# Kernel optimization log

Measured on AMD Instinct MI355X. Metric: run time of the kernel, lower is better.

Reference implementation:

```python
import jax, jax.numpy as jnp
import numpy as np

BN_EPS = 1e-5


def setup_inputs() -> dict:
    key = jax.random.key(0)
    ks = jax.random.split(key, 8)
    B, C, N = 4, 256, 4096
    s = 1.0 / np.sqrt(C)
    return {
        "feature": jax.random.normal(ks[0], (B, C, N, 1), dtype=jnp.float32),
        "Wa": jax.random.normal(ks[1], (C, C), dtype=jnp.float32) * s,
        "ba": jnp.zeros((C,), dtype=jnp.float32),
        "Wb": jax.random.normal(ks[2], (C, C), dtype=jnp.float32) * s,
        "bb": jnp.zeros((C,), dtype=jnp.float32),
        "Wm": jax.random.normal(ks[3], (C, C), dtype=jnp.float32) * s,
        "bm": jnp.zeros((C,), dtype=jnp.float32),
        "gamma": jnp.ones((C,), dtype=jnp.float32),
        "beta": jnp.zeros((C,), dtype=jnp.float32),
        "rmean": jnp.zeros((C,), dtype=jnp.float32),
        "rvar": jnp.ones((C,), dtype=jnp.float32),
        "alpha": jnp.zeros((1,), dtype=jnp.float32),
    }


def reference(feature, Wa, ba, Wb, bb, Wm, bm, gamma, beta, rmean, rvar, alpha):
    # feature: [B, C, N, 1]; 1x1 convs are per-point linear maps over channels.
    x = feature[..., 0]  # [B, C, N]
    a = jnp.einsum('oc,bcn->bon', Wa, x) + ba[None, :, None]  # fc_a
    b = jnp.einsum('oc,bcn->bon', Wb, x) + bb[None, :, None]  # fc_b
    # att = softmax(a^T @ b) over last dim: [B, N, N]
    att = jax.nn.softmax(jnp.einsum('bcn,bcm->bnm', a, b), axis=2)
    # mlp: 1x1 conv + eval-mode BatchNorm
    m = jnp.einsum('oc,bcn->bon', Wm, x) + bm[None, :, None]
    inv = jax.lax.rsqrt(rvar + BN_EPS)
    m = (m - rmean[None, :, None]) * (inv * gamma)[None, :, None] + beta[None, :, None]
    # f = att @ m^T -> [B, N, C], back to [B, C, N]
    f = jnp.einsum('bnm,bcm->bcn', att, m)
    return feature + alpha[0] * f[..., None]
```

## Files before the change

### kernel.cpp

```cpp
#include <hip/hip_runtime.h>
#include <hip/hip_bf16.h>

typedef __bf16 bf16x8 __attribute__((ext_vector_type(8)));
typedef float f32x4 __attribute__((ext_vector_type(4)));
typedef float f32x16 __attribute__((ext_vector_type(16)));
typedef int i32x4 __attribute__((ext_vector_type(4)));
typedef int i32x8 __attribute__((ext_vector_type(8)));
typedef unsigned int u32;

#define MFMA16 __builtin_amdgcn_mfma_f32_16x16x32_bf16
#define MFMASC(a, b, c) \
  __builtin_amdgcn_mfma_scale_f32_32x32x64_f8f6f4((a), (b), (c), 0, 0, 0, 0x7F7F7F7F, 0, 0x7F7F7F7F)

#define LOG2E 1.44269504f

__device__ __forceinline__ unsigned short f2b(float f) {
  return __builtin_bit_cast(unsigned short, (__bf16)f);
}

__device__ __forceinline__ u32 pk4(float a, float b, float c, float d) {
  int v = __builtin_amdgcn_cvt_pk_fp8_f32(a, b, 0, false);
  v = __builtin_amdgcn_cvt_pk_fp8_f32(c, d, v, true);
  return (u32)v;
}

__device__ __forceinline__ void gload_lds16(const void* g, void* l) {
  __builtin_amdgcn_global_load_lds(
      (const __attribute__((address_space(1))) unsigned int*)g,
      (__attribute__((address_space(3))) unsigned int*)l, 16, 0, 0);
}

__global__ __launch_bounds__(256) void k_wconv(const float* __restrict__ Wa,
                                               const float* __restrict__ Wb,
                                               const float* __restrict__ Wm,
                                               unsigned short* __restrict__ W16) {
  const int m = blockIdx.y;
  const float* W = (m == 0) ? Wa : (m == 1) ? Wb : Wm;
  const int i = (blockIdx.x * 256 + threadIdx.x) * 8;
  float4 a = *reinterpret_cast<const float4*>(W + i);
  float4 b = *reinterpret_cast<const float4*>(W + i + 4);
  ushort4 lo, hi;
  lo.x = f2b(a.x); lo.y = f2b(a.y); lo.z = f2b(a.z); lo.w = f2b(a.w);
  hi.x = f2b(b.x); hi.y = f2b(b.y); hi.z = f2b(b.z); hi.w = f2b(b.w);
  unsigned short* dst = W16 + m * 65536 + i;
  *reinterpret_cast<ushort4*>(dst) = lo;
  *reinterpret_cast<ushort4*>(dst + 4) = hi;
}

__global__ __launch_bounds__(256) void k_proj(
    const float* __restrict__ x, const unsigned short* __restrict__ W16,
    const float* __restrict__ ba, const float* __restrict__ bb,
    const float* __restrict__ bm, const float* __restrict__ gamma,
    const float* __restrict__ beta, const float* __restrict__ rmean,
    const float* __restrict__ rvar,
    unsigned char* __restrict__ Q8, unsigned char* __restrict__ K8,
    unsigned char* __restrict__ V8) {
  __shared__ float tile[256][36];
  __shared__ __align__(16) unsigned short XT_lds[32 * 256];
  const int nt = blockIdx.x, b = blockIdx.y;
  const int n0 = nt * 32;
  const int tid = threadIdx.x, w = tid >> 6, l = tid & 63;
  const int li = l & 15, lk = l >> 4;
  {
    const int cr = tid >> 3, j4 = (tid & 7) * 4;
#pragma unroll
    for (int p = 0; p < 8; ++p) {
      int c = p * 32 + cr;
      float4 v = *reinterpret_cast<const float4*>(
          x + ((size_t)(b * 256 + c)) * 4096 + n0 + j4);
      *reinterpret_cast<float4*>(&tile[c][j4]) = v;
    }
  }
  __syncthreads();
  {
    const int n = tid & 31, cb8 = (tid >> 5) * 32;
#pragma unroll
    for (int p = 0; p < 8; ++p) {
      int c0 = cb8 + p * 4;
      ushort4 o;
      o.x = f2b(tile[c0][n]); o.y = f2b(tile[c0 + 1][n]);
      o.z = f2b(tile[c0 + 2][n]); o.w = f2b(tile[c0 + 3][n]);
      unsigned off = ((unsigned)(n * 512 + c0 * 2)) ^ (unsigned)((n & 7) << 4);
      *reinterpret_cast<ushort4*>((char*)XT_lds + off) = o;
    }
  }
  __syncthreads();
  bf16x8 af[2][8];
#pragma unroll
  for (int rs = 0; rs < 2; ++rs) {
    const int row = rs * 16 + li;
#pragma unroll
    for (int kk = 0; kk < 8; ++kk) {
      unsigned off = ((unsigned)(row * 512 + kk * 64 + lk * 16)) ^ (unsigned)((row & 7) << 4);
      af[rs][kk] = *reinterpret_cast<const bf16x8*>((const char*)XT_lds + off);
    }
  }
  const int ofb = w * 4;
  f32x4 zero = {0.f, 0.f, 0.f, 0.f};
  f32x4 acc[2][4];
  {
#pragma unroll
    for (int rs = 0; rs < 2; ++rs)
#pragma unroll
      for (int i = 0; i < 4; ++i) acc[rs][i] = zero;
#pragma unroll
    for (int kk = 0; kk < 8; ++kk)
#pragma unroll
      for (int of = 0; of < 4; ++of) {
        bf16x8 bfv = *reinterpret_cast<const bf16x8*>(
            W16 + (size_t)((ofb + of) * 16 + li) * 256 + kk * 32 + lk * 8);
        acc[0][of] = MFMA16(bfv, af[0][kk], acc[0][of], 0, 0, 0);
        acc[1][of] = MFMA16(bfv, af[1][kk], acc[1][of], 0, 0, 0);
      }
#pragma unroll
    for (int rs = 0; rs < 2; ++rs) {
      const int n = n0 + rs * 16 + li;
      unsigned char* out = Q8 + ((size_t)b * 4096 + n) * 256;
#pragma unroll
      for (int of = 0; of < 4; ++of) {
        int c0 = (ofb + of) * 16 + lk * 4;
        float4 bs = *reinterpret_cast<const float4*>(ba + c0);
        u32 v = pk4((acc[rs][of][0] + bs.x) * LOG2E, (acc[rs][of][1] + bs.y) * LOG2E,
                    (acc[rs][of][2] + bs.z) * LOG2E, (acc[rs][of][3] + bs.w) * LOG2E);
        *reinterpret_cast<u32*>(out + c0) = v;
      }
    }
  }
  {
#pragma unroll
    for (int rs = 0; rs < 2; ++rs)
#pragma unroll
      for (int i = 0; i < 4; ++i) acc[rs][i] = zero;
#pragma unroll
    for (int kk = 0; kk < 8; ++kk)
#pragma unroll
      for (int of = 0; of < 4; ++of) {
        bf16x8 bfv = *reinterpret_cast<const bf16x8*>(
            W16 + 65536 + (size_t)((ofb + of) * 16 + li) * 256 + kk * 32 + lk * 8);
        acc[0][of] = MFMA16(bfv, af[0][kk], acc[0][of], 0, 0, 0);
        acc[1][of] = MFMA16(bfv, af[1][kk], acc[1][of], 0, 0, 0);
      }
#pragma unroll
    for (int rs = 0; rs < 2; ++rs) {
      const int n = n0 + rs * 16 + li;
      unsigned char* out = K8 + ((size_t)b * 4096 + n) * 256;
#pragma unroll
      for (int of = 0; of < 4; ++of) {
        int c0 = (ofb + of) * 16 + lk * 4;
        float4 bs = *reinterpret_cast<const float4*>(bb + c0);
        u32 v = pk4(acc[rs][of][0] + bs.x, acc[rs][of][1] + bs.y,
                    acc[rs][of][2] + bs.z, acc[rs][of][3] + bs.w);
        *reinterpret_cast<u32*>(out + c0) = v;
      }
    }
  }
  {
#pragma unroll
    for (int rs = 0; rs < 2; ++rs)
#pragma unroll
      for (int i = 0; i < 4; ++i) acc[rs][i] = zero;
#pragma unroll
    for (int kk = 0; kk < 8; ++kk)
#pragma unroll
      for (int of = 0; of < 4; ++of) {
        bf16x8 bfv = *reinterpret_cast<const bf16x8*>(
            W16 + 131072 + (size_t)((ofb + of) * 16 + li) * 256 + kk * 32 + lk * 8);
        acc[0][of] = MFMA16(af[0][kk], bfv, acc[0][of], 0, 0, 0);
        acc[1][of] = MFMA16(af[1][kk], bfv, acc[1][of], 0, 0, 0);
      }
#pragma unroll
    for (int of = 0; of < 4; ++of) {
      int c = (ofb + of) * 16 + li;
      float g = rsqrtf(rvar[c] + 1e-5f) * gamma[c];
      float sh = (bm[c] - rmean[c]) * g + beta[c];
#pragma unroll
      for (int rs = 0; rs < 2; ++rs) {
        const int nn0 = n0 + rs * 16 + lk * 4;
        u32 v = pk4(acc[rs][of][0] * g + sh, acc[rs][of][1] * g + sh,
                    acc[rs][of][2] * g + sh, acc[rs][of][3] * g + sh);
        *reinterpret_cast<u32*>(
            V8 + ((size_t)b * 128 + (nn0 >> 5)) * 8192 + c * 32 + (nn0 & 31)) = v;
      }
    }
  }
}

__global__ __launch_bounds__(256, 2) void k_attn(
    const unsigned char* __restrict__ Q8, const unsigned char* __restrict__ K8,
    const unsigned char* __restrict__ V8, unsigned short* __restrict__ part,
    float* __restrict__ mpart, float* __restrict__ lpart) {
  __shared__ __align__(32) unsigned char K_lds[64 * 256];
  __shared__ __align__(32) unsigned char V_lds[2 * 8192];
  const int bid = blockIdx.x;
  const int swz = (bid & 7) * 64 + (bid >> 3);
  const int qt = swz & 31;
  const int bs = swz >> 5;
  const int b = bs >> 2, s = bs & 3;
  const int tid = threadIdx.x, w = tid >> 6, l = tid & 63;
  const int q = l & 31, hi = l >> 5;
  const int rowq = qt * 128 + w * 32 + q;
  i32x8 qf8[4];
  const unsigned char* qp = Q8 + ((size_t)b * 4096 + rowq) * 256 + hi * 32;
#pragma unroll
  for (int kk = 0; kk < 4; ++kk)
    qf8[kk] = *reinterpret_cast<const i32x8*>(qp + kk * 64);
  f32x16 acc[8];
#pragma unroll
  for (int i = 0; i < 8; ++i)
#pragma unroll
    for (int r = 0; r < 16; ++r) acc[i][r] = 0.f;
  float mr = -3e38f, lr = 0.f;

  const int kbase = s * 1024;
  auto stageK = [&](int t) {
#pragma unroll
    for (int g = 0; g < 4; ++g) {
      int row = w * 16 + g * 4 + (l >> 4);
      int c16 = (l & 15) ^ ((row & 7) << 1);
      const unsigned char* src =
          K8 + ((size_t)b * 4096 + kbase + t * 64 + row) * 256 + c16 * 16;
      gload_lds16(src, &K_lds[(w * 16 + g * 4) * 256]);
    }
  };
  auto stageV = [&](int t) {
    const unsigned char* base =
        V8 + ((size_t)b * 128 + (kbase >> 5) + t * 2) * 8192;
#pragma unroll
    for (int g = 0; g < 4; ++g)
      gload_lds16(base + (g * 4 + w) * 1024 + l * 16, &V_lds[(g * 4 + w) * 1024]);
  };

  stageK(0);
  stageV(0);
  asm volatile("s_waitcnt vmcnt(0)" ::: "memory");
  __syncthreads();
  for (int t = 0; t < 16; ++t) {
    f32x16 S0, S1;
#pragma unroll
    for (int r = 0; r < 16; ++r) { S0[r] = 0.f; S1[r] = 0.f; }
    __builtin_amdgcn_s_setprio(1);
#pragma unroll
    for (int kk = 0; kk < 4; ++kk) {
      int off = (((kk * 2 + hi) ^ (q & 7)) << 5);
      i32x8 kf0 = *reinterpret_cast<const i32x8*>(&K_lds[q * 256 + off]);
      i32x8 kf1 = *reinterpret_cast<const i32x8*>(&K_lds[(32 + q) * 256 + off]);
      S0 = MFMASC(kf0, qf8[kk], S0);
      S1 = MFMASC(kf1, qf8[kk], S1);
    }
    __builtin_amdgcn_s_setprio(0);
    float m0 = fmaxf(S0[0], S1[0]), m1 = fmaxf(S0[1], S1[1]);
    float m2 = fmaxf(S0[2], S1[2]), m3 = fmaxf(S0[3], S1[3]);
#pragma unroll
    for (int r = 4; r < 16; r += 4) {
      m0 = fmaxf(m0, fmaxf(S0[r + 0], S1[r + 0]));
      m1 = fmaxf(m1, fmaxf(S0[r + 1], S1[r + 1]));
      m2 = fmaxf(m2, fmaxf(S0[r + 2], S1[r + 2]));
      m3 = fmaxf(m3, fmaxf(S0[r + 3], S1[r + 3]));
    }
    float pmax = fmaxf(fmaxf(m0, m1), fmaxf(m2, m3));
    pmax = fmaxf(pmax, __shfl_xor(pmax, 32));
    if (!__all(pmax - mr <= 7.0f)) {
      float nm = fmaxf(mr, pmax);
      float sc = exp2f(mr - nm);
      mr = nm;
      lr *= sc;
#pragma unroll
      for (int cb = 0; cb < 8; ++cb)
#pragma unroll
        for (int r = 0; r < 16; ++r) acc[cb][r] *= sc;
    }
#pragma unroll
    for (int r = 0; r < 16; ++r) { S0[r] = exp2f(S0[r] - mr); S1[r] = exp2f(S1[r] - mr); }
    float s0_ = S0[0] + S1[0], s1_ = S0[1] + S1[1];
    float s2_ = S0[2] + S1[2], s3_ = S0[3] + S1[3];
#pragma unroll
    for (int r = 4; r < 16; r += 4) {
      s0_ += S0[r + 0] + S1[r + 0];
      s1_ += S0[r + 1] + S1[r + 1];
      s2_ += S0[r + 2] + S1[r + 2];
      s3_ += S0[r + 3] + S1[r + 3];
    }
    float sum = (s0_ + s1_) + (s2_ + s3_);
    sum += __shfl_xor(sum, 32);
    lr += sum;
    u32 A0 = pk4(S0[0], S0[1], S0[2], S0[3]);
    u32 A1 = pk4(S0[4], S0[5], S0[6], S0[7]);
    u32 A2 = pk4(S0[8], S0[9], S0[10], S0[11]);
    u32 A3 = pk4(S0[12], S0[13], S0[14], S0[15]);
    u32 B0 = pk4(S1[0], S1[1], S1[2], S1[3]);
    u32 B1 = pk4(S1[4], S1[5], S1[6], S1[7]);
    u32 B2 = pk4(S1[8], S1[9], S1[10], S1[11]);
    u32 B3 = pk4(S1[12], S1[13], S1[14], S1[15]);
    asm volatile("v_permlane32_swap_b32 %0, %1" : "+v"(A0), "+v"(B0));
    asm volatile("v_permlane32_swap_b32 %0, %1" : "+v"(A1), "+v"(B1));
    asm volatile("v_permlane32_swap_b32 %0, %1" : "+v"(A2), "+v"(B2));
    asm volatile("v_permlane32_swap_b32 %0, %1" : "+v"(A3), "+v"(B3));
    i32x8 pb = (i32x8){(int)A0, (int)B0, (int)A1, (int)B1,
                       (int)A2, (int)B2, (int)A3, (int)B3};
    __builtin_amdgcn_s_setprio(1);
#pragma unroll
    for (int cb = 0; cb < 8; ++cb) {
      i32x8 vf = *reinterpret_cast<const i32x8*>(
          &V_lds[hi * 8192 + (cb * 32 + q) * 32]);
      acc[cb] = MFMASC(vf, pb, acc[cb]);
    }
    __builtin_amdgcn_s_setprio(0);
    if (t + 1 < 16) {
      __syncthreads();
      stageK(t + 1);
      stageV(t + 1);
      asm volatile("s_waitcnt vmcnt(0)" ::: "memory");
      __syncthreads();
    }
  }
  const int sb = s * 4 + b;
  size_t pbase = ((size_t)sb * 4096 + rowq) * 256;
#pragma unroll
  for (int cb = 0; cb < 8; ++cb)
#pragma unroll
    for (int g = 0; g < 4; ++g) {
      ushort4 o;
      o.x = f2b(acc[cb][g * 4 + 0]); o.y = f2b(acc[cb][g * 4 + 1]);
      o.z = f2b(acc[cb][g * 4 + 2]); o.w = f2b(acc[cb][g * 4 + 3]);
      *reinterpret_cast<ushort4*>(&part[pbase + cb * 32 + g * 8 + hi * 4]) = o;
    }
  if (hi == 0) {
    mpart[sb * 4096 + rowq] = mr;
    lpart[sb * 4096 + rowq] = lr;
  }
}

__global__ __launch_bounds__(256) void k_comb(
    const unsigned short* __restrict__ part, const float* __restrict__ mpart,
    const float* __restrict__ lpart, const float* __restrict__ feat,
    const float* __restrict__ alpha, float* __restrict__ out) {
  __shared__ float wgt[4][32];
  __shared__ float tile[32][261];
  const int nt = blockIdx.x, b = blockIdx.y;
  const int n0 = nt * 32;
  const int tid = threadIdx.x;
  if (tid < 32) {
    int qn = n0 + tid;
    float m[4], lv[4];
#pragma unroll
    for (int s = 0; s < 4; ++s) {
      m[s] = mpart[(s * 4 + b) * 4096 + qn];
      lv[s] = lpart[(s * 4 + b) * 4096 + qn];
    }
    float M = fmaxf(fmaxf(m[0], m[1]), fmaxf(m[2], m[3]));
    float e[4], L = 0.f;
#pragma unroll
    for (int s = 0; s < 4; ++s) { e[s] = exp2f(m[s] - M); L += e[s] * lv[s]; }
    float inv = 1.0f / L;
#pragma unroll
    for (int s = 0; s < 4; ++s) wgt[s][tid] = e[s] * inv;
  }
  __syncthreads();
  const int row = tid >> 3;
  const int c0 = (tid & 7) * 32;
  float acc[32];
#pragma unroll
  for (int k = 0; k < 32; ++k) acc[k] = 0.f;
#pragma unroll
  for (int s = 0; s < 4; ++s) {
    float ww = wgt[s][row];
    const unsigned short* p = part + (((size_t)(s * 4 + b)) * 4096 + n0 + row) * 256 + c0;
#pragma unroll
    for (int ch = 0; ch < 4; ++ch) {
      bf16x8 v = *reinterpret_cast<const bf16x8*>(p + ch * 8);
#pragma unroll
      for (int j = 0; j < 8; ++j) acc[ch * 8 + j] += ww * (float)v[j];
    }
  }
#pragma unroll
  for (int k = 0; k < 32; ++k) tile[row][c0 + k] = acc[k];
  __syncthreads();
  const float av = alpha[0];
  const int j = tid & 7, cb = tid >> 3;
#pragma unroll
  for (int p = 0; p < 8; ++p) {
    int c = cb * 8 + p;
    size_t gbase = ((size_t)(b * 256 + c)) * 4096 + n0 + j * 4;
    float4 f4 = *reinterpret_cast<const float4*>(feat + gbase);
    float4 o;
    o.x = f4.x + av * tile[j * 4 + 0][c];
    o.y = f4.y + av * tile[j * 4 + 1][c];
    o.z = f4.z + av * tile[j * 4 + 2][c];
    o.w = f4.w + av * tile[j * 4 + 3][c];
    *reinterpret_cast<float4*>(out + gbase) = o;
  }
}

extern "C" void kernel_launch(void* const* d_in, const int* in_sizes, int n_in,
                              void* d_out, int out_size, void* d_ws, size_t ws_size,
                              hipStream_t stream) {
  const float* feat  = (const float*)d_in[0];
  const float* Wa    = (const float*)d_in[1];
  const float* ba    = (const float*)d_in[2];
  const float* Wb    = (const float*)d_in[3];
  const float* bb    = (const float*)d_in[4];
  const float* Wm    = (const float*)d_in[5];
  const float* bm    = (const float*)d_in[6];
  const float* gamma = (const float*)d_in[7];
  const float* beta  = (const float*)d_in[8];
  const float* rmean = (const float*)d_in[9];
  const float* rvar  = (const float*)d_in[10];
  const float* alpha = (const float*)d_in[11];
  float* out = (float*)d_out;
  char* ws = (char*)d_ws;
  unsigned char*  Q8   = (unsigned char*)(ws);
  unsigned char*  K8   = (unsigned char*)(ws + ((size_t)4 << 20));
  unsigned char*  V8   = (unsigned char*)(ws + ((size_t)8 << 20));
  unsigned short* part = (unsigned short*)(ws + ((size_t)16 << 20));
  unsigned short* W16  = (unsigned short*)(ws + ((size_t)48 << 20));
  float* mpart = (float*)(ws + ((size_t)48 << 20) + 393216);
  float* lpart = (float*)(ws + ((size_t)48 << 20) + 393216 + 262144);

  k_wconv<<<dim3(32, 3), 256, 0, stream>>>(Wa, Wb, Wm, W16);
  k_proj<<<dim3(128, 4), 256, 0, stream>>>(feat, W16, ba, bb, bm, gamma, beta,
                                           rmean, rvar, Q8, K8, V8);
  k_attn<<<dim3(512), 256, 0, stream>>>(Q8, K8, V8, part, mpart, lpart);
  k_comb<<<dim3(128, 4), 256, 0, stream>>>(part, mpart, lpart, feat, alpha, out);
}
```

Measured before the change: 115.7 us.

## Double-buffer V in LDS and prefetch next K/V tile during softmax

```diff
diff --git a/kernel.cpp b/kernel.cpp
--- a/kernel.cpp
+++ b/kernel.cpp
@@ -190,7 +190,7 @@
     const unsigned char* __restrict__ V8, unsigned short* __restrict__ part,
     float* __restrict__ mpart, float* __restrict__ lpart) {
   __shared__ __align__(32) unsigned char K_lds[64 * 256];
-  __shared__ __align__(32) unsigned char V_lds[2 * 8192];
+  __shared__ __align__(32) unsigned char V_lds[2][2 * 8192];
   const int bid = blockIdx.x;
   const int swz = (bid & 7) * 64 + (bid >> 3);
   const int qt = swz & 31;
@@ -222,18 +222,19 @@
       gload_lds16(src, &K_lds[(w * 16 + g * 4) * 256]);
     }
   };
-  auto stageV = [&](int t) {
+  auto stageV = [&](int buf, int t) {
     const unsigned char* base =
         V8 + ((size_t)b * 128 + (kbase >> 5) + t * 2) * 8192;
 #pragma unroll
     for (int g = 0; g < 4; ++g)
-      gload_lds16(base + (g * 4 + w) * 1024 + l * 16, &V_lds[(g * 4 + w) * 1024]);
+      gload_lds16(base + (g * 4 + w) * 1024 + l * 16, &V_lds[buf][(g * 4 + w) * 1024]);
   };
 
   stageK(0);
-  stageV(0);
+  stageV(0, 0);
   asm volatile("s_waitcnt vmcnt(0)" ::: "memory");
   __syncthreads();
+  int cur = 0;
   for (int t = 0; t < 16; ++t) {
     f32x16 S0, S1;
 #pragma unroll
@@ -248,16 +249,28 @@
       S1 = MFMASC(kf1, qf8[kk], S1);
     }
     __builtin_amdgcn_s_setprio(0);
-    float m0 = fmaxf(S0[0], S1[0]), m1 = fmaxf(S0[1], S1[1]);
-    float m2 = fmaxf(S0[2], S1[2]), m3 = fmaxf(S0[3], S1[3]);
-#pragma unroll
-    for (int r = 4; r < 16; r += 4) {
-      m0 = fmaxf(m0, fmaxf(S0[r + 0], S1[r + 0]));
-      m1 = fmaxf(m1, fmaxf(S0[r + 1], S1[r + 1]));
-      m2 = fmaxf(m2, fmaxf(S0[r + 2], S1[r + 2]));
-      m3 = fmaxf(m3, fmaxf(S0[r + 3], S1[r + 3]));
-    }
-    float pmax = fmaxf(fmaxf(m0, m1), fmaxf(m2, m3));
+    if (t + 1 < 16) {
+      __syncthreads();
+      stageK(t + 1);
+      stageV(cur ^ 1, t + 1);
+    }
+    float m0 = fmaxf(fmaxf(S0[0], S1[0]), S0[4]);
+    m0 = fmaxf(fmaxf(m0, S1[4]), S0[8]);
+    m0 = fmaxf(fmaxf(m0, S1[8]), S0[12]);
+    m0 = fmaxf(m0, S1[12]);
+    float m1 = fmaxf(fmaxf(S0[1], S1[1]), S0[5]);
+    m1 = fmaxf(fmaxf(m1, S1[5]), S0[9]);
+    m1 = fmaxf(fmaxf(m1, S1[9]), S0[13]);
+    m1 = fmaxf(m1, S1[13]);
+    float m2 = fmaxf(fmaxf(S0[2], S1[2]), S0[6]);
+    m2 = fmaxf(fmaxf(m2, S1[6]), S0[10]);
+    m2 = fmaxf(fmaxf(m2, S1[10]), S0[14]);
+    m2 = fmaxf(m2, S1[14]);
+    float m3 = fmaxf(fmaxf(S0[3], S1[3]), S0[7]);
+    m3 = fmaxf(fmaxf(m3, S1[7]), S0[11]);
+    m3 = fmaxf(fmaxf(m3, S1[11]), S0[15]);
+    m3 = fmaxf(m3, S1[15]);
+    float pmax = fmaxf(fmaxf(fmaxf(m0, m1), m2), m3);
     pmax = fmaxf(pmax, __shfl_xor(pmax, 32));
     if (!__all(pmax - mr <= 7.0f)) {
       float nm = fmaxf(mr, pmax);
@@ -301,16 +314,14 @@
 #pragma unroll
     for (int cb = 0; cb < 8; ++cb) {
       i32x8 vf = *reinterpret_cast<const i32x8*>(
-          &V_lds[hi * 8192 + (cb * 32 + q) * 32]);
+          &V_lds[cur][hi * 8192 + (cb * 32 + q) * 32]);
       acc[cb] = MFMASC(vf, pb, acc[cb]);
     }
     __builtin_amdgcn_s_setprio(0);
     if (t + 1 < 16) {
-      __syncthreads();
-      stageK(t + 1);
-      stageV(t + 1);
       asm volatile("s_waitcnt vmcnt(0)" ::: "memory");
       __syncthreads();
+      cur ^= 1;
     }
   }
   const int sb = s * 4 + b;
```

After: 114.5 us. About the same (-1.0%).
